# Kernel tuning notes

Measured on AMD Instinct MI355X. Metric: run time of the kernel, lower is better.

## Reference

```python
import jax, jax.numpy as jnp
import numpy as np

T_DIL = 10   # neighbor-count threshold
K_DIL = 2    # skip hyperparameter
BN_EPS = 1e-5
NORM_EPS = 1e-12


def _dilate_pattern(adj_bool, mask_b):
    """Sequential (row-by-row) dilated neighbor skipping on a [N,N] bool adjacency.
    Faithful to the torch double loop: earlier rows' removals (including the
    symmetric column zeroing) affect later rows' neighbor sets."""
    N = adj_bool.shape[0]

    def step(carry, n):
        row = jnp.take(carry, n, axis=0)                 # [N] bool, current neighbors of n
        nbi = row.astype(jnp.int32)
        num = jnp.sum(nbi)
        sf = jnp.where(num > T_DIL, (num + K_DIL - 1) // K_DIL, 1)  # linear mode, ceil(num/k)
        rank = jnp.cumsum(nbi)                           # 1-based rank among neighbors
        rm = row & ((rank % sf) == 0)                    # neighbors[sf-1::sf]
        valid = (mask_b[n] != 0) & (num > 1)
        rm = jnp.where(valid, rm, False)
        keep = ~rm
        carry = carry.at[n].set(row & keep)              # adj[n, to_remove] = 0
        carry = carry.at[:, n].set(carry[:, n] & keep)   # adj[to_remove, n] = 0
        return carry, None

    out, _ = jax.lax.scan(step, adj_bool, jnp.arange(N))
    return out


def _dilate(adj, mask):
    # keep-pattern is piecewise constant in adj; multiply so removed entries -> 0
    keep = jax.vmap(_dilate_pattern)(adj > 0, mask)
    return adj * keep.astype(adj.dtype)


def _sage(x, adj, Wr, Wx, b, mf):
    # DenseSAGEConv: mean-aggregate, lin_rel + lin_root, L2 normalize, mask
    deg = jnp.clip(jnp.sum(adj, axis=-1, keepdims=True), 1.0, None)
    agg = jnp.einsum('bij,bjd->bid', adj, x) / deg
    out = agg @ Wr + x @ Wx + b
    nrm = jnp.maximum(jnp.linalg.norm(out, axis=-1, keepdims=True), NORM_EPS)
    return (out / nrm) * mf[..., None]


def _bn(x, g, b):
    # BatchNorm1d in training mode over flattened (B*N) rows, biased variance
    m = jnp.mean(x, axis=(0, 1))
    v = jnp.var(x, axis=(0, 1))
    return (x - m) * jax.lax.rsqrt(v + BN_EPS) * g + b


def _forward(x, adj, mask, Wr1, Wx1, b1, g1, be1, Wr2, Wx2, b2, g2, be2,
             Wr3, Wx3, b3, g3, be3, Wl, bl):
    mf = mask.astype(x.dtype)
    # linear dilation mode: skip factor is layer-independent, and each layer
    # dilates the ORIGINAL adj (torch clones adj per call) -> compute once
    adj_d = _dilate(adj, mask)
    h1 = _bn(jax.nn.relu(_sage(x, adj_d, Wr1, Wx1, b1, mf)), g1, be1)
    h2 = _bn(jax.nn.relu(_sage(h1, adj_d, Wr2, Wx2, b2, mf)), g2, be2)
    h3 = _bn(jax.nn.relu(_sage(h2, adj_d, Wr3, Wx3, b3, mf)), g3, be3)
    xc = jnp.concatenate([h1, h2, h3], axis=-1) * mf[..., None]
    return (xc @ Wl + bl) * mf[..., None]


def setup_inputs() -> dict:
    B, N, D, H, E = 8, 2048, 128, 128, 128
    key = jax.random.key(0)
    ks = jax.random.split(key, 24)
    x = jax.random.normal(ks[0], (B, N, D), dtype=jnp.float32)
    a = jax.random.bernoulli(ks[1], 0.01, (B, N, N))
    a = a | jnp.swapaxes(a, 1, 2)
    a = a & ~jnp.eye(N, dtype=bool)[None]
    adj = a.astype(jnp.float32)
    mask = jnp.ones((B, N), dtype=jnp.int32)
    s = 0.05
    p = {}
    dims = [(D, H), (H, H), (H, E)]
    for i, (di, do) in enumerate(dims, 1):
        p[f'Wr{i}'] = s * jax.random.normal(ks[2 * i], (di, do), dtype=jnp.float32)
        p[f'Wx{i}'] = s * jax.random.normal(ks[2 * i + 1], (di, do), dtype=jnp.float32)
        p[f'b{i}'] = jnp.zeros((do,), dtype=jnp.float32)
        p[f'g{i}'] = jnp.ones((do,), dtype=jnp.float32)
        p[f'be{i}'] = jnp.zeros((do,), dtype=jnp.float32)
    p['Wl'] = s * jax.random.normal(ks[10], (2 * H + E, E), dtype=jnp.float32)
    p['bl'] = jnp.zeros((E,), dtype=jnp.float32)
    return {'x': x, 'adj': adj, 'mask': mask, **p}


def reference(x, adj, mask, Wr1, Wx1, b1, g1, be1, Wr2, Wx2, b2, g2, be2,
              Wr3, Wx3, b3, g3, be3, Wl, bl):
    return _forward(x, adj, mask, Wr1, Wx1, b1, g1, be1, Wr2, Wx2, b2, g2, be2,
                    Wr3, Wx3, b3, g3, be3, Wl, bl)
```

## Files before the change

kernel.cpp:

```cpp
#include <hip/hip_runtime.h>
#include <cstdint>

constexpr int B_ = 8, N_ = 2048, D_ = 128, NW = 64;
constexpr int EMAX = 131072;
constexpr int RPS = 2064;
constexpr int TDIL = 10;

constexpr size_t OFF_BITSET = 0;
constexpr size_t OFF_AGG    = 0;
constexpr size_t OFF_H1     = (size_t)8  << 20;
constexpr size_t OFF_H2     = (size_t)16 << 20;
constexpr size_t OFF_H3     = (size_t)24 << 20;
constexpr size_t OFF_XB     = (size_t)24 << 20;
constexpr size_t OFF_H1B    = (size_t)28 << 20;
constexpr size_t OFF_H2B    = (size_t)24 << 20;
constexpr size_t OFF_COLS   = (size_t)32 << 20;
constexpr size_t OFF_PACKED = (size_t)34 << 20;
constexpr size_t OFF_RP     = (size_t)38 << 20;
constexpr size_t OFF_DEG0   = OFF_RP   + ((size_t)128 << 10);
constexpr size_t OFF_DEGF   = OFF_DEG0 + ((size_t)64  << 10);
constexpr size_t OFF_BN     = OFF_DEGF + ((size_t)64  << 10);
constexpr size_t OFF_WHI    = OFF_BN  + ((size_t)4 << 10);
constexpr size_t OFF_WLO    = OFF_WHI + ((size_t)304 << 10);

typedef __attribute__((ext_vector_type(8))) short short8v;
typedef __attribute__((ext_vector_type(4))) float f32x4;

__device__ __forceinline__ uint16_t bf16rne(float f) {
    uint32_t u = __float_as_uint(f);
    return (uint16_t)((u + 0x7FFFu + ((u >> 16) & 1u)) >> 16);
}

__global__ __launch_bounds__(256) void kW_prep(
        const float* __restrict__ Wr1, const float* __restrict__ Wx1,
        const float* __restrict__ Wr2, const float* __restrict__ Wx2,
        const float* __restrict__ Wr3, const float* __restrict__ Wx3,
        const float* __restrict__ Wl,
        uint16_t* __restrict__ whi, uint16_t* __restrict__ wlo,
        float* __restrict__ bn,
        const float* __restrict__ x, uint16_t* __restrict__ xb) {
    if (blockIdx.x >= 128) {
        size_t i = ((size_t)(blockIdx.x - 128) * 256 + threadIdx.x) * 4;
        float4 v = *(const float4*)&x[i];
        ushort4 o;
        o.x = bf16rne(v.x); o.y = bf16rne(v.y);
        o.z = bf16rne(v.z); o.w = bf16rne(v.w);
        *(ushort4*)&xb[i] = o;
        return;
    }
    if (blockIdx.x == 0) {
        for (int i = threadIdx.x; i < 768; i += 256) bn[i] = 0.f;
    }
    int g  = blockIdx.x >> 5;
    int lb = blockIdx.x & 31;
    int K = (g == 3) ? 384 : 256;
    const float* A  = (g == 0) ? Wr1 : (g == 1) ? Wr2 : (g == 2) ? Wr3 : Wl;
    const float* Bw = (g == 0) ? Wx1 : (g == 1) ? Wx2 : (g == 2) ? Wx3 : nullptr;
    size_t base = (g == 3) ? (size_t)98304 : (size_t)g * 32768;
    int total = K * 128;
    for (int f = lb * 256 + threadIdx.x; f < total; f += 32 * 256) {
        int e = f & 7, lane = (f >> 3) & 63, ct = (f >> 9) & 7, ks = f >> 12;
        int k = ks * 32 + ((lane >> 4) << 3) + e;
        int col = (ct << 4) + (lane & 15);
        float v = (g == 3 || k < 128) ? A[(size_t)k * 128 + col]
                                      : Bw[(size_t)(k - 128) * 128 + col];
        uint32_t hi = bf16rne(v);
        float hf = __uint_as_float(hi << 16);
        whi[base + f] = (uint16_t)hi;
        wlo[base + f] = bf16rne(v - hf);
    }
}

__global__ __launch_bounds__(256) void k1_bitset(const float* __restrict__ adj,
        uint32_t* __restrict__ bitset, uint32_t* __restrict__ deg0) {
    int row  = blockIdx.x * 4 + (threadIdx.x >> 6);
    int lane = threadIdx.x & 63;
    const float* ar = adj + (size_t)row * N_;
    uint32_t myw = 0;
    #pragma unroll 4
    for (int it = 0; it < 32; ++it) {
        float v = ar[it * 64 + lane];
        unsigned long long m = __ballot(v != 0.0f);
        if (lane == 2 * it)          myw = (uint32_t)m;
        else if (lane == 2 * it + 1) myw = (uint32_t)(m >> 32);
    }
    bitset[(size_t)row * NW + lane] = myw;
    int pc = __popc(myw);
    #pragma unroll
    for (int off = 32; off >= 1; off >>= 1) pc += __shfl_xor(pc, off);
    if (lane == 0) deg0[row] = (uint32_t)pc;
}

__global__ __launch_bounds__(256) void k2_rowptr(const uint32_t* __restrict__ deg0,
        uint32_t* __restrict__ rowptr) {
    int b = blockIdx.x, t = threadIdx.x;
    __shared__ uint32_t tsum[256];
    uint32_t v[8]; uint32_t s = 0;
    #pragma unroll
    for (int j = 0; j < 8; ++j) { v[j] = deg0[b * N_ + t * 8 + j]; s += v[j]; v[j] = s; }
    tsum[t] = s;
    __syncthreads();
    for (int off = 1; off < 256; off <<= 1) {
        uint32_t xv = (t >= off) ? tsum[t - off] : 0u;
        __syncthreads();
        tsum[t] += xv;
        __syncthreads();
    }
    uint32_t excl = tsum[t] - s;
    uint32_t* rp = rowptr + (size_t)b * RPS;
    if (t == 0) rp[0] = 0;
    #pragma unroll
    for (int j = 0; j < 8; ++j) {
        uint32_t val = excl + v[j];
        if (val > (uint32_t)EMAX) val = EMAX;
        rp[t * 8 + j + 1] = val;
    }
}

__global__ __launch_bounds__(256) void k3_cols(const uint32_t* __restrict__ bitset,
        const uint32_t* __restrict__ rowptr, uint16_t* __restrict__ cols) {
    int row  = blockIdx.x * 4 + (threadIdx.x >> 6);
    int lane = threadIdx.x & 63;
    int b = row >> 11, n = row & (N_ - 1);
    uint32_t w = bitset[(size_t)row * NW + lane];
    uint32_t pc = __popc(w);
    uint32_t inc = pc;
    #pragma unroll
    for (int off = 1; off < 64; off <<= 1) {
        uint32_t t = __shfl_up(inc, off);
        if (lane >= off) inc += t;
    }
    uint32_t base = rowptr[(size_t)b * RPS + n] + (inc - pc);
    uint16_t* cb = cols + (size_t)b * EMAX;
    while (w) {
        int bit = __builtin_ctz(w); w &= w - 1;
        if (base < (uint32_t)EMAX) cb[base] = (uint16_t)(lane * 32 + bit);
        ++base;
    }
}

__global__ __launch_bounds__(256) void k4_packed(const uint16_t* __restrict__ cols,
        const uint32_t* __restrict__ rowptr, uint32_t* __restrict__ packed) {
    int row  = blockIdx.x * 4 + (threadIdx.x >> 6);
    int lane = threadIdx.x & 63;
    int b = row >> 11, n = row & (N_ - 1);
    const uint32_t* rpb = rowptr + (size_t)b * RPS;
    const uint16_t* cb  = cols + (size_t)b * EMAX;
    uint32_t start = rpb[n], end = rpb[n + 1];
    for (uint32_t e = start + lane; e < end; e += 64) {
        uint32_t j = cb[e];
        uint32_t lo = rpb[j], hi = rpb[j + 1];
        uint32_t rj = lo;
        while (lo < hi) {
            uint32_t mid = (lo + hi) >> 1;
            if ((int)cb[mid] < n) lo = mid + 1; else hi = mid;
        }
        packed[(size_t)b * EMAX + e] = j | ((lo - rj) << 16);
    }
}

#define K5_ISSUE(PK0, PK1, CNT, ROW)                                        \
    do {                                                                    \
        int rr_ = (ROW);                                                    \
        if (rr_ < N_) {                                                     \
            uint32_t ldI_ = rps[rr_], enI_ = rps[rr_ + 1];                  \
            CNT = (int)(enI_ - ldI_);                                       \
            PK0 = (lane < CNT) ? pkg[ldI_ + lane] : 0xFFFFFFFFu;            \
            if (CNT > 64)                                                   \
                PK1 = (lane + 64 < CNT) ? pkg[ldI_ + 64 + lane] : 0xFFFFFFFFu; \
            else PK1 = 0xFFFFFFFFu;                                         \
        } else { CNT = 0; PK0 = 0xFFFFFFFFu; PK1 = 0xFFFFFFFFu; }           \
    } while (0)

#define K5_PROC(PK0, PK1, CNT, NROW)                                        \
    do {                                                                    \
        int nr_ = (NROW);                                                   \
        if (CNT <= 64) {                                                    \
                            \
            uint32_t c0_ = PK0 & 0xFFFFu;                                   \
            bool e0_ = (lane < CNT) && (c0_ < (uint32_t)nr_);               \
            while (true) {                                                  \
                uint32_t d0_ = e0_ ? __hip_atomic_load(&done[c0_ >> 5],     \
                        __ATOMIC_ACQUIRE, __HIP_MEMORY_SCOPE_WORKGROUP) : 0u; \
                bool ok0_ = !e0_ || ((d0_ >> (c0_ & 31)) & 1u);             \
                if (__all((int)ok0_)) break;                                \
            }                                                               \
            __builtin_amdgcn_s_setprio(1);                                  \
            uint2 mc_ = *(const uint2*)&rm4[(size_t)nr_ * 4];               \
            uint32_t w01_ = (lane < 32) ? mc_.x : mc_.y;                    \
            uint32_t a0_ = (w01_ >> (lane & 31)) & 1u;                      \
            unsigned long long bl0_ = __ballot(a0_ != 0);                   \
            uint32_t num_ = (uint32_t)__popcll(bl0_);                       \
            if (mk[nr_] && num_ > 1u) {                                     \
                bool allrm_ = num_ <= (uint32_t)TDIL;                       \
                uint32_t sf_ = (num_ + 1u) >> 1;                            \
                uint32_t r2_ = (num_ & 1u) ? 0xFFFFFFFFu : num_;            \
                uint32_t rank0_ = (uint32_t)__popcll(bl0_ & below) + 1u;    \
                bool rm0_ = a0_ && (allrm_ || rank0_ == sf_ || rank0_ == r2_); \
                unsigned long long rb0_ = __ballot(rm0_);                   \
                if (rm0_) {                                                 \
                    uint32_t ml_ = PK0 >> 16;                               \
                    if (ml_ < 128u) atomicAnd(&rm4[c0_ * 4 + (ml_ >> 5)], ~(1u << (ml_ & 31))); \
                }                                                           \
                if (lane == 0) {                                            \
                    uint2 nm_;                                              \
                    nm_.x = mc_.x & ~(uint32_t)rb0_;                        \
                    nm_.y = mc_.y & ~(uint32_t)(rb0_ >> 32);                \
                    *(uint2*)&rm4[(size_t)nr_ * 4] = nm_;                   \
                }                                                           \
            }                                                               \
            __asm__ __volatile__("" ::: "memory");                          \
            if (lane == 0)                                                  \
                __hip_atomic_fetch_or(&done[nr_ >> 5], 1u << (nr_ & 31),    \
                        __ATOMIC_RELAXED, __HIP_MEMORY_SCOPE_WORKGROUP);    \
            __builtin_amdgcn_s_setprio(0);                                  \
        } else {                                                            \
                      \
            uint32_t c0_ = PK0 & 0xFFFFu, c1_ = PK1 & 0xFFFFu;              \
            bool e0_ = (lane < CNT)      && (c0_ < (uint32_t)nr_);          \
            bool e1_ = (lane + 64 < CNT) && (c1_ < (uint32_t)nr_);          \
            while (true) {                                                  \
                uint32_t d0_ = e0_ ? __hip_atomic_load(&done[c0_ >> 5],     \
                        __ATOMIC_ACQUIRE, __HIP_MEMORY_SCOPE_WORKGROUP) : 0u; \
                uint32_t d1_ = e1_ ? __hip_atomic_load(&done[c1_ >> 5],     \
                        __ATOMIC_ACQUIRE, __HIP_MEMORY_SCOPE_WORKGROUP) : 0u; \
                bool ok0_ = !e0_ || ((d0_ >> (c0_ & 31)) & 1u);             \
                bool ok1_ = !e1_ || ((d1_ >> (c1_ & 31)) & 1u);             \
                if (__all((int)(ok0_ && ok1_))) break;                      \
            }                                                               \
            __builtin_amdgcn_s_setprio(1);                                  \
            uint4 mcur_ = *(const uint4*)&rm4[(size_t)nr_ * 4];             \
            uint32_t w01_ = (lane < 32) ? mcur_.x : mcur_.y;                \
            uint32_t w23_ = (lane < 32) ? mcur_.z : mcur_.w;                \
            uint32_t a0_ = (w01_ >> (lane & 31)) & 1u;                      \
            uint32_t a1_ = (w23_ >> (lane & 31)) & 1u;                      \
            unsigned long long bl0_ = __ballot(a0_ != 0), bl1_ = __ballot(a1_ != 0); \
            uint32_t num_ = (uint32_t)__popcll(bl0_) + (uint32_t)__popcll(bl1_); \
            if (mk[nr_] && num_ > 1u) {                                     \
                bool allrm_ = num_ <= (uint32_t)TDIL;                       \
                uint32_t sf_ = (num_ + 1u) >> 1;                            \
                uint32_t r2_ = (num_ & 1u) ? 0xFFFFFFFFu : num_;            \
                uint32_t rank0_ = (uint32_t)__popcll(bl0_ & below) + 1u;    \
                uint32_t rank1_ = (uint32_t)__popcll(bl0_) +                \
                                  (uint32_t)__popcll(bl1_ & below) + 1u;    \
                bool rm0_ = a0_ && (allrm_ || rank0_ == sf_ || rank0_ == r2_); \
                bool rm1_ = a1_ && (allrm_ || rank1_ == sf_ || rank1_ == r2_); \
                unsigned long long rb0_ = __ballot(rm0_), rb1_ = __ballot(rm1_); \
                if (rm0_) {                                                 \
                    uint32_t ml_ = PK0 >> 16;                               \
                    if (ml_ < 128u) atomicAnd(&rm4[c0_ * 4 + (ml_ >> 5)], ~(1u << (ml_ & 31))); \
                }                                                           \
                if (rm1_) {                                                 \
                    uint32_t ml_ = PK1 >> 16;                               \
                    if (ml_ < 128u) atomicAnd(&rm4[c1_ * 4 + (ml_ >> 5)], ~(1u << (ml_ & 31))); \
                }                                                           \
                if (lane == 0) {                                            \
                    uint4 nm_;                                              \
                    nm_.x = mcur_.x & ~(uint32_t)rb0_;                      \
                    nm_.y = mcur_.y & ~(uint32_t)(rb0_ >> 32);              \
                    nm_.z = mcur_.z & ~(uint32_t)rb1_;                      \
                    nm_.w = mcur_.w & ~(uint32_t)(rb1_ >> 32);              \
                    *(uint4*)&rm4[(size_t)nr_ * 4] = nm_;                   \
                }                                                           \
            }                                                               \
            __asm__ __volatile__("" ::: "memory");                          \
            if (lane == 0)                                                  \
                __hip_atomic_fetch_or(&done[nr_ >> 5], 1u << (nr_ & 31),    \
                        __ATOMIC_RELAXED, __HIP_MEMORY_SCOPE_WORKGROUP);    \
            __builtin_amdgcn_s_setprio(0);                                  \
        }                                                                   \
    } while (0)

__global__ __launch_bounds__(1024) void k5_fused(
        const uint32_t* __restrict__ packed, const uint32_t* __restrict__ rowptr,
        const uint32_t* __restrict__ deg0, const int* __restrict__ mask,
        uint16_t* __restrict__ cols, uint32_t* __restrict__ degf) {
    int b = blockIdx.x;
    int tid = threadIdx.x;
    int lane = tid & 63;
    int wv = tid >> 6;
    __shared__ __align__(16) uint32_t rm4[N_ * 4];
    __shared__ uint32_t rps[N_ + 1];
    __shared__ uint8_t  mk[N_];
    __shared__ uint32_t done[64];
    const uint32_t* pkg = packed + (size_t)b * EMAX;
    const uint32_t* rpg = rowptr + (size_t)b * RPS;
    uint16_t* cbm = cols + (size_t)b * EMAX;

    for (int i = tid; i <= N_; i += 1024) rps[i] = rpg[i];
    if (tid < 64) done[tid] = 0u;
    for (int i = tid; i < N_; i += 1024) {
        int d = (int)deg0[b * N_ + i]; if (d > 128) d = 128;
        uint4 mm;
        mm.x = (d >= 32) ? ~0u : ((d > 0)  ? ((1u << d)        - 1u) : 0u);
        mm.y = (d >= 64) ? ~0u : ((d > 32) ? ((1u << (d - 32)) - 1u) : 0u);
        mm.z = (d >= 96) ? ~0u : ((d > 64) ? ((1u << (d - 64)) - 1u) : 0u);
        mm.w = (d >= 128)? ~0u : ((d > 96) ? ((1u << (d - 96)) - 1u) : 0u);
        *(uint4*)&rm4[(size_t)i * 4] = mm;
        mk[i] = (uint8_t)(mask[b * N_ + i] != 0);
    }
    __syncthreads();

    unsigned long long below = (1ULL << lane) - 1ULL;
    int cntA, cntB, cntC;
    uint32_t pkA0, pkA1, pkB0, pkB1, pkC0, pkC1;
    K5_ISSUE(pkA0, pkA1, cntA, wv);
    K5_ISSUE(pkB0, pkB1, cntB, wv + 16);
    K5_ISSUE(pkC0, pkC1, cntC, wv + 32);

    int n = wv;
    while (n < N_) {
        K5_PROC(pkA0, pkA1, cntA, n);
        K5_ISSUE(pkA0, pkA1, cntA, n + 48);
        n += 16; if (n >= N_) break;
        K5_PROC(pkB0, pkB1, cntB, n);
        K5_ISSUE(pkB0, pkB1, cntB, n + 48);
        n += 16; if (n >= N_) break;
        K5_PROC(pkC0, pkC1, cntC, n);
        K5_ISSUE(pkC0, pkC1, cntC, n + 48);
        n += 16;
    }
    __syncthreads();

    for (int i = wv; i < N_; i += 16) {
        uint4 mm = *(const uint4*)&rm4[(size_t)i * 4];
        if (lane == 0)
            degf[b * N_ + i] = (uint32_t)(__popc(mm.x) + __popc(mm.y) +
                                          __popc(mm.z) + __popc(mm.w));
        uint32_t st = rps[i];
        uint32_t w01 = (lane < 32) ? mm.x : mm.y;
        uint32_t w23 = (lane < 32) ? mm.z : mm.w;
        uint32_t a0 = (w01 >> (lane & 31)) & 1u;
        uint32_t a1 = (w23 >> (lane & 31)) & 1u;
        unsigned long long b0 = __ballot(a0 != 0), b1v = __ballot(a1 != 0);
        uint16_t c0v = 0, c1v = 0;
        if (a0) c0v = cbm[st + lane];
        if (a1) c1v = cbm[st + 64 + lane];
        uint32_t i0 = st + (uint32_t)__popcll(b0 & below);
        uint32_t i1 = st + (uint32_t)__popcll(b0) + (uint32_t)__popcll(b1v & below);
        if (a0) cbm[i0] = c0v;
        if (a1) cbm[i1] = c1v;
    }
}

__global__ __launch_bounds__(256) void k7_spmm(const uint16_t* __restrict__ Xb16,
        const uint16_t* __restrict__ cols, const uint32_t* __restrict__ rowptr,
        const uint32_t* __restrict__ degf, float* __restrict__ agg) {
    int wid  = blockIdx.x * 4 + (threadIdx.x >> 6);
    int lane = threadIdx.x & 63;
    int b = wid >> 11, n = wid & (N_ - 1);
    const uint16_t* cb = cols + (size_t)b * EMAX;
    uint32_t start = rowptr[(size_t)b * RPS + n];
    uint32_t cnt = degf[wid];
    const uint16_t* Xb = Xb16 + ((size_t)b * N_) * D_;
    float ax = 0.f, ay = 0.f;
    for (uint32_t base = 0; base < cnt; base += 64) {
        int idx = (int)base + lane;
        int cl = (idx < (int)cnt) ? (int)cb[start + idx] : 0;
        int kmax = (int)cnt - (int)base; if (kmax > 64) kmax = 64;
        int k = 0;
        for (; k + 4 <= kmax; k += 4) {
            int cA = __shfl(cl, k),     cB = __shfl(cl, k + 1);
            int cC = __shfl(cl, k + 2), cD = __shfl(cl, k + 3);
            uint32_t uA = ((const uint32_t*)(Xb + (size_t)cA * D_))[lane];
            uint32_t uB = ((const uint32_t*)(Xb + (size_t)cB * D_))[lane];
            uint32_t uC = ((const uint32_t*)(Xb + (size_t)cC * D_))[lane];
            uint32_t uD = ((const uint32_t*)(Xb + (size_t)cD * D_))[lane];
            ax += __uint_as_float(uA << 16) + __uint_as_float(uB << 16)
                + __uint_as_float(uC << 16) + __uint_as_float(uD << 16);
            ay += __uint_as_float(uA & 0xFFFF0000u) + __uint_as_float(uB & 0xFFFF0000u)
                + __uint_as_float(uC & 0xFFFF0000u) + __uint_as_float(uD & 0xFFFF0000u);
        }
        for (; k < kmax; ++k) {
            int c = __shfl(cl, k);
            uint32_t u = ((const uint32_t*)(Xb + (size_t)c * D_))[lane];
            ax += __uint_as_float(u << 16);
            ay += __uint_as_float(u & 0xFFFF0000u);
        }
    }
    float inv = 1.0f / (float)(cnt ? cnt : 1u);
    ((float2*)(agg + (size_t)wid * D_))[lane] = make_float2(ax * inv, ay * inv);
}

__device__ __forceinline__ void cvt_store4(uint16_t* hiA, uint16_t* loA,
                                           int idx, float4 v) {
    float vv[4] = {v.x, v.y, v.z, v.w};
    ushort4 hs, ls;
    uint16_t* hp = (uint16_t*)&hs; uint16_t* lp = (uint16_t*)&ls;
    #pragma unroll
    for (int i = 0; i < 4; ++i) {
        uint32_t hi = bf16rne(vv[i]);
        float hf = __uint_as_float(hi << 16);
        hp[i] = (uint16_t)hi;
        lp[i] = bf16rne(vv[i] - hf);
    }
    *(ushort4*)&hiA[idx] = hs;
    *(ushort4*)&loA[idx] = ls;
}

constexpr int ASTR = 264;
__global__ __launch_bounds__(256) void k8_mfma(const float* __restrict__ agg,
        const float* __restrict__ Hin,
        const uint16_t* __restrict__ whi, const uint16_t* __restrict__ wlo,
        const float* __restrict__ bias, const int* __restrict__ mask,
        const float* __restrict__ bnp, const float* __restrict__ gp,
        const float* __restrict__ bep, int use_bn,
        float* __restrict__ P, uint16_t* __restrict__ Pb,
        float* __restrict__ bnstat) {
    __shared__ __align__(16) char buf[2 * 32 * ASTR * 2];
    __shared__ float scL[128], shL[128];
    uint16_t* aHi = (uint16_t*)buf;
    uint16_t* aLo = (uint16_t*)(buf + 32 * ASTR * 2);
    float* outP = (float*)buf;
    int tid = threadIdx.x, lane = tid & 63, h = tid >> 6;
    size_t row0 = (size_t)blockIdx.x * 32;

    if (tid < 128) {
        float sc = 1.f, sh = 0.f;
        if (use_bn) {
            float mean = bnp[tid] * (1.f / 16384.f);
            float var  = bnp[128 + tid] * (1.f / 16384.f) - mean * mean;
            sc = gp[tid] * rsqrtf(var + 1e-5f);
            sh = bep[tid] - mean * sc;
        }
        scL[tid] = sc; shL[tid] = sh;
    }
    __syncthreads();

    for (int f = tid * 4; f < 4096; f += 1024) {
        int r = f >> 7, c = f & 127;
        float4 va = *(const float4*)&agg[(row0 + r) * 128 + c];
        float4 vx = *(const float4*)&Hin[(row0 + r) * 128 + c];
        float4 s4 = *(const float4*)&scL[c];
        float4 h4 = *(const float4*)&shL[c];
        va.x = va.x * s4.x + h4.x; va.y = va.y * s4.y + h4.y;
        va.z = va.z * s4.z + h4.z; va.w = va.w * s4.w + h4.w;
        vx.x = vx.x * s4.x + h4.x; vx.y = vx.y * s4.y + h4.y;
        vx.z = vx.z * s4.z + h4.z; vx.w = vx.w * s4.w + h4.w;
        cvt_store4(aHi, aLo, r * ASTR + c, va);
        cvt_store4(aHi, aLo, r * ASTR + 128 + c, vx);
    }
    __syncthreads();

    f32x4 acc00 = {0.f,0.f,0.f,0.f}, acc01 = acc00, acc10 = acc00, acc11 = acc00;
    int ct0 = h * 2, ct1 = h * 2 + 1;
    int arow = (lane & 15);
    int koff = (lane >> 4) * 8;
    #pragma unroll
    for (int ks = 0; ks < 8; ++ks) {
        int k0 = ks * 32 + koff;
        short8v a0h = *(short8v*)&aHi[arow * ASTR + k0];
        short8v a0l = *(short8v*)&aLo[arow * ASTR + k0];
        short8v a1h = *(short8v*)&aHi[(arow + 16) * ASTR + k0];
        short8v a1l = *(short8v*)&aLo[(arow + 16) * ASTR + k0];
        short8v b0h = *(const short8v*)&whi[(size_t)(((ks * 8 + ct0) << 6) + lane) * 8];
        short8v b0l = *(const short8v*)&wlo[(size_t)(((ks * 8 + ct0) << 6) + lane) * 8];
        short8v b1h = *(const short8v*)&whi[(size_t)(((ks * 8 + ct1) << 6) + lane) * 8];
        short8v b1l = *(const short8v*)&wlo[(size_t)(((ks * 8 + ct1) << 6) + lane) * 8];
        acc00 = __builtin_amdgcn_mfma_f32_16x16x32_bf16(a0h, b0h, acc00, 0, 0, 0);
        acc00 = __builtin_amdgcn_mfma_f32_16x16x32_bf16(a0h, b0l, acc00, 0, 0, 0);
        acc00 = __builtin_amdgcn_mfma_f32_16x16x32_bf16(a0l, b0h, acc00, 0, 0, 0);
        acc01 = __builtin_amdgcn_mfma_f32_16x16x32_bf16(a0h, b1h, acc01, 0, 0, 0);
        acc01 = __builtin_amdgcn_mfma_f32_16x16x32_bf16(a0h, b1l, acc01, 0, 0, 0);
        acc01 = __builtin_amdgcn_mfma_f32_16x16x32_bf16(a0l, b1h, acc01, 0, 0, 0);
        acc10 = __builtin_amdgcn_mfma_f32_16x16x32_bf16(a1h, b0h, acc10, 0, 0, 0);
        acc10 = __builtin_amdgcn_mfma_f32_16x16x32_bf16(a1h, b0l, acc10, 0, 0, 0);
        acc10 = __builtin_amdgcn_mfma_f32_16x16x32_bf16(a1l, b0h, acc10, 0, 0, 0);
        acc11 = __builtin_amdgcn_mfma_f32_16x16x32_bf16(a1h, b1h, acc11, 0, 0, 0);
        acc11 = __builtin_amdgcn_mfma_f32_16x16x32_bf16(a1h, b1l, acc11, 0, 0, 0);
        acc11 = __builtin_amdgcn_mfma_f32_16x16x32_bf16(a1l, b1h, acc11, 0, 0, 0);
    }
    __syncthreads();

    int orow = (lane >> 4) * 4;
    int oc0 = ct0 * 16 + (lane & 15);
    int oc1 = ct1 * 16 + (lane & 15);
    #pragma unroll
    for (int j = 0; j < 4; ++j) {
        outP[(orow + j) * 128 + oc0]      = acc00[j];
        outP[(orow + j) * 128 + oc1]      = acc01[j];
        outP[(16 + orow + j) * 128 + oc0] = acc10[j];
        outP[(16 + orow + j) * 128 + oc1] = acc11[j];
    }
    __syncthreads();

    float bs0 = bias[lane], bs1 = bias[lane + 64];
    #pragma unroll
    for (int i = 0; i < 8; ++i) {
        int r = h * 8 + i;
        float v0 = outP[r * 128 + lane] + bs0;
        float v1 = outP[r * 128 + lane + 64] + bs1;
        float s = v0 * v0 + v1 * v1;
        #pragma unroll
        for (int off = 32; off >= 1; off >>= 1) s += __shfl_xor(s, off);
        float nrm = fmaxf(sqrtf(s), 1e-12f);
        float mf = (mask[row0 + r] != 0) ? 1.f : 0.f;
        float inv = mf / nrm;
        float p0 = fmaxf(v0 * inv, 0.f), p1 = fmaxf(v1 * inv, 0.f);
        P[(row0 + r) * 128 + lane]      = p0;
        P[(row0 + r) * 128 + lane + 64] = p1;
        if (Pb) {
            Pb[(row0 + r) * 128 + lane]      = bf16rne(p0);
            Pb[(row0 + r) * 128 + lane + 64] = bf16rne(p1);
        }
        outP[r * 128 + lane] = p0; outP[r * 128 + lane + 64] = p1;
    }
    __syncthreads();
    if (tid < 128) {
        float s = 0.f, q = 0.f;
        #pragma unroll
        for (int r = 0; r < 32; ++r) { float v = outP[r * 128 + tid]; s += v; q += v * v; }
        atomicAdd(&bnstat[tid], s);
        atomicAdd(&bnstat[128 + tid], q);
    }
}

__global__ __launch_bounds__(256) void k11_final(const float* __restrict__ h1,
        const float* __restrict__ h2, const float* __restrict__ h3,
        const float* __restrict__ Wl, const float* __restrict__ bl,
        const int* __restrict__ mask, const float* __restrict__ bn,
        const float* __restrict__ g1, const float* __restrict__ be1,
        const float* __restrict__ g2, const float* __restrict__ be2,
        const float* __restrict__ g3, const float* __restrict__ be3,
        float* __restrict__ out) {
    __shared__ float s1[32 * 128], s2[32 * 128], s3[32 * 128];
    __shared__ float scA[128], shA[128], scB[128], shB[128], scC[128], shC[128];
    int tid = threadIdx.x;
    size_t row0 = (size_t)blockIdx.x * 32;
    if (tid < 128) {
        float m1 = bn[tid] * (1.f / 16384.f);
        float v1 = bn[128 + tid] * (1.f / 16384.f) - m1 * m1;
        scA[tid] = g1[tid] * rsqrtf(v1 + 1e-5f);
        shA[tid] = be1[tid] - m1 * scA[tid];
        float m2 = bn[256 + tid] * (1.f / 16384.f);
        float v2 = bn[384 + tid] * (1.f / 16384.f) - m2 * m2;
        scB[tid] = g2[tid] * rsqrtf(v2 + 1e-5f);
        shB[tid] = be2[tid] - m2 * scB[tid];
        float m3 = bn[512 + tid] * (1.f / 16384.f);
        float v3 = bn[640 + tid] * (1.f / 16384.f) - m3 * m3;
        scC[tid] = g3[tid] * rsqrtf(v3 + 1e-5f);
        shC[tid] = be3[tid] - m3 * scC[tid];
    }
    __syncthreads();
    for (int t = tid * 4; t < 32 * 128; t += 1024) {
        int r = t >> 7;
        float mf = (mask[row0 + r] != 0) ? 1.f : 0.f;
        int c = t & 127;
        float4 a = *(const float4*)&h1[row0 * 128 + t];
        float4 b = *(const float4*)&h2[row0 * 128 + t];
        float4 cc = *(const float4*)&h3[row0 * 128 + t];
        float4 sa = *(const float4*)&scA[c], ha = *(const float4*)&shA[c];
        float4 sb = *(const float4*)&scB[c], hb = *(const float4*)&shB[c];
        float4 sc = *(const float4*)&scC[c], hc = *(const float4*)&shC[c];
        a.x = (a.x * sa.x + ha.x) * mf; a.y = (a.y * sa.y + ha.y) * mf;
        a.z = (a.z * sa.z + ha.z) * mf; a.w = (a.w * sa.w + ha.w) * mf;
        b.x = (b.x * sb.x + hb.x) * mf; b.y = (b.y * sb.y + hb.y) * mf;
        b.z = (b.z * sb.z + hb.z) * mf; b.w = (b.w * sb.w + hb.w) * mf;
        cc.x = (cc.x * sc.x + hc.x) * mf; cc.y = (cc.y * sc.y + hc.y) * mf;
        cc.z = (cc.z * sc.z + hc.z) * mf; cc.w = (cc.w * sc.w + hc.w) * mf;
        *(float4*)&s1[t] = a; *(float4*)&s2[t] = b; *(float4*)&s3[t] = cc;
    }
    __syncthreads();
    int h = tid >> 6, c0 = (tid & 63) * 2;
    float2 acc[8];
    #pragma unroll
    for (int i = 0; i < 8; ++i) acc[i] = make_float2(0.f, 0.f);
    for (int k4 = 0; k4 < 128; k4 += 4) {
        float2 w1[4], w2[4], w3[4];
        #pragma unroll
        for (int kk = 0; kk < 4; ++kk) {
            w1[kk] = *(const float2*)&Wl[(k4 + kk) * 128 + c0];
            w2[kk] = *(const float2*)&Wl[(128 + k4 + kk) * 128 + c0];
            w3[kk] = *(const float2*)&Wl[(256 + k4 + kk) * 128 + c0];
        }
        #pragma unroll
        for (int i = 0; i < 8; ++i) {
            int r = h * 8 + i;
            float4 a = *(const float4*)&s1[r * 128 + k4];
            float4 b = *(const float4*)&s2[r * 128 + k4];
            float4 c = *(const float4*)&s3[r * 128 + k4];
            acc[i].x += a.x * w1[0].x + a.y * w1[1].x + a.z * w1[2].x + a.w * w1[3].x
                      + b.x * w2[0].x + b.y * w2[1].x + b.z * w2[2].x + b.w * w2[3].x
                      + c.x * w3[0].x + c.y * w3[1].x + c.z * w3[2].x + c.w * w3[3].x;
            acc[i].y += a.x * w1[0].y + a.y * w1[1].y + a.z * w1[2].y + a.w * w1[3].y
                      + b.x * w2[0].y + b.y * w2[1].y + b.z * w2[2].y + b.w * w2[3].y
                      + c.x * w3[0].y + c.y * w3[1].y + c.z * w3[2].y + c.w * w3[3].y;
        }
    }
    float bx = bl[c0], by = bl[c0 + 1];
    #pragma unroll
    for (int i = 0; i < 8; ++i) {
        int r = h * 8 + i;
        float mf = (mask[row0 + r] != 0) ? 1.f : 0.f;
        *(float2*)&out[(row0 + r) * 128 + c0] =
            make_float2((acc[i].x + bx) * mf, (acc[i].y + by) * mf);
    }
}

extern "C" void kernel_launch(void* const* d_in, const int* in_sizes, int n_in,
                              void* d_out, int out_size, void* d_ws, size_t ws_size,
                              hipStream_t stream) {
    (void)in_sizes; (void)n_in; (void)out_size; (void)ws_size;
    const float* x    = (const float*)d_in[0];
    const float* adj  = (const float*)d_in[1];
    const int*   mask = (const int*)d_in[2];
    const float* Wr1 = (const float*)d_in[3],  *Wx1 = (const float*)d_in[4];
    const float* b1  = (const float*)d_in[5],  *g1  = (const float*)d_in[6],  *be1 = (const float*)d_in[7];
    const float* Wr2 = (const float*)d_in[8],  *Wx2 = (const float*)d_in[9];
    const float* b2  = (const float*)d_in[10], *g2  = (const float*)d_in[11], *be2 = (const float*)d_in[12];
    const float* Wr3 = (const float*)d_in[13], *Wx3 = (const float*)d_in[14];
    const float* b3  = (const float*)d_in[15], *g3  = (const float*)d_in[16], *be3 = (const float*)d_in[17];
    const float* Wl  = (const float*)d_in[18], *bl  = (const float*)d_in[19];

    char* ws = (char*)d_ws;
    uint32_t* bitset = (uint32_t*)(ws + OFF_BITSET);
    float*    agg    = (float*)(ws + OFF_AGG);
    float*    h1     = (float*)(ws + OFF_H1);
    float*    h2     = (float*)(ws + OFF_H2);
    float*    h3     = (float*)(ws + OFF_H3);
    uint16_t* xb     = (uint16_t*)(ws + OFF_XB);
    uint16_t* h1b    = (uint16_t*)(ws + OFF_H1B);
    uint16_t* h2b    = (uint16_t*)(ws + OFF_H2B);
    uint16_t* cols   = (uint16_t*)(ws + OFF_COLS);
    uint32_t* packed = (uint32_t*)(ws + OFF_PACKED);
    uint32_t* rp     = (uint32_t*)(ws + OFF_RP);
    uint32_t* deg0   = (uint32_t*)(ws + OFF_DEG0);
    uint32_t* degf   = (uint32_t*)(ws + OFF_DEGF);
    float*    bn     = (float*)(ws + OFF_BN);
    uint16_t* whi    = (uint16_t*)(ws + OFF_WHI);
    uint16_t* wlo    = (uint16_t*)(ws + OFF_WLO);
    float*    out    = (float*)d_out;

    kW_prep   <<<2176, 256, 0, stream>>>(Wr1, Wx1, Wr2, Wx2, Wr3, Wx3, Wl,
                                         whi, wlo, bn, x, xb);
    k1_bitset <<<4096, 256, 0, stream>>>(adj, bitset, deg0);
    k2_rowptr <<<8,    256, 0, stream>>>(deg0, rp);
    k3_cols   <<<4096, 256, 0, stream>>>(bitset, rp, cols);
    k4_packed <<<4096, 256, 0, stream>>>(cols, rp, packed);
    k5_fused  <<<8,    1024, 0, stream>>>(packed, rp, deg0, mask, cols, degf);
    k7_spmm   <<<4096, 256, 0, stream>>>(xb,  cols, rp, degf, agg);
    k8_mfma   <<<512,  256, 0, stream>>>(agg, x,  whi,         wlo,         b1, mask,
                                         bn, g1, be1, 0, h1, h1b, bn + 0);
    k7_spmm   <<<4096, 256, 0, stream>>>(h1b, cols, rp, degf, agg);
    k8_mfma   <<<512,  256, 0, stream>>>(agg, h1, whi + 32768, wlo + 32768, b2, mask,
                                         bn + 0, g1, be1, 1, h2, h2b, bn + 256);
    k7_spmm   <<<4096, 256, 0, stream>>>(h2b, cols, rp, degf, agg);
    k8_mfma   <<<512,  256, 0, stream>>>(agg, h2, whi + 65536, wlo + 65536, b3, mask,
                                         bn + 256, g2, be2, 1, h3, nullptr, bn + 512);
    k11_final <<<512,  256, 0, stream>>>(h1, h2, h3, Wl, bl, mask, bn,
                                         g1, be1, g2, be2, g3, be3, out);
}
```

Measured before the change: 330.3 us.

## Replace column compaction in dilate kernel with per-row keep bitmask consumed by SpMM

The dilate kernel no longer compacts the surviving columns into the CSR column array. It writes each row's 128-bit keep mask to global memory, and the SpMM kernel walks the original CSR row while skipping entries whose mask bit is clear. This removes the serial-ish compaction tail from the single-block-per-batch dilate kernel. The cost is that the SpMM inner loop loses its 4-way unrolling and now runs a per-entry branch over the undilated degree, three times.

After: 359.3 us. 1.09x slower.

```diff
diff --git a/kernel.cpp b/kernel.cpp
--- a/kernel.cpp
+++ b/kernel.cpp
@@ -19,7 +19,8 @@
 constexpr size_t OFF_RP     = (size_t)38 << 20;
 constexpr size_t OFF_DEG0   = OFF_RP   + ((size_t)128 << 10);
 constexpr size_t OFF_DEGF   = OFF_DEG0 + ((size_t)64  << 10);
-constexpr size_t OFF_BN     = OFF_DEGF + ((size_t)64  << 10);
+constexpr size_t OFF_RMASK  = OFF_DEGF + ((size_t)64  << 10);
+constexpr size_t OFF_BN     = OFF_RMASK + ((size_t)256 << 10);
 constexpr size_t OFF_WHI    = OFF_BN  + ((size_t)4 << 10);
 constexpr size_t OFF_WLO    = OFF_WHI + ((size_t)304 << 10);
 
@@ -271,10 +272,10 @@
         }                                                                   \
     } while (0)
 
-__global__ __launch_bounds__(1024) void k5_fused(
+__global__ __launch_bounds__(1024) void k5_dilate(
         const uint32_t* __restrict__ packed, const uint32_t* __restrict__ rowptr,
         const uint32_t* __restrict__ deg0, const int* __restrict__ mask,
-        uint16_t* __restrict__ cols, uint32_t* __restrict__ degf) {
+        uint32_t* __restrict__ rmaskg, uint32_t* __restrict__ degf) {
     int b = blockIdx.x;
     int tid = threadIdx.x;
     int lane = tid & 63;
@@ -285,7 +286,6 @@
     __shared__ uint32_t done[64];
     const uint32_t* pkg = packed + (size_t)b * EMAX;
     const uint32_t* rpg = rowptr + (size_t)b * RPS;
-    uint16_t* cbm = cols + (size_t)b * EMAX;
 
     for (int i = tid; i <= N_; i += 1024) rps[i] = rpg[i];
     if (tid < 64) done[tid] = 0u;
@@ -321,63 +321,44 @@
         n += 16;
     }
     __syncthreads();
-
-    for (int i = wv; i < N_; i += 16) {
+    for (int i = tid; i < N_; i += 1024) {
         uint4 mm = *(const uint4*)&rm4[(size_t)i * 4];
-        if (lane == 0)
-            degf[b * N_ + i] = (uint32_t)(__popc(mm.x) + __popc(mm.y) +
-                                          __popc(mm.z) + __popc(mm.w));
-        uint32_t st = rps[i];
-        uint32_t w01 = (lane < 32) ? mm.x : mm.y;
-        uint32_t w23 = (lane < 32) ? mm.z : mm.w;
-        uint32_t a0 = (w01 >> (lane & 31)) & 1u;
-        uint32_t a1 = (w23 >> (lane & 31)) & 1u;
-        unsigned long long b0 = __ballot(a0 != 0), b1v = __ballot(a1 != 0);
-        uint16_t c0v = 0, c1v = 0;
-        if (a0) c0v = cbm[st + lane];
-        if (a1) c1v = cbm[st + 64 + lane];
-        uint32_t i0 = st + (uint32_t)__popcll(b0 & below);
-        uint32_t i1 = st + (uint32_t)__popcll(b0) + (uint32_t)__popcll(b1v & below);
-        if (a0) cbm[i0] = c0v;
-        if (a1) cbm[i1] = c1v;
+        *(uint4*)&rmaskg[((size_t)b * N_ + i) * 4] = mm;
+        degf[b * N_ + i] = (uint32_t)(__popc(mm.x) + __popc(mm.y) + __popc(mm.z) + __popc(mm.w));
     }
 }
 
 __global__ __launch_bounds__(256) void k7_spmm(const uint16_t* __restrict__ Xb16,
         const uint16_t* __restrict__ cols, const uint32_t* __restrict__ rowptr,
-        const uint32_t* __restrict__ degf, float* __restrict__ agg) {
+        const uint32_t* __restrict__ rmaskg, const uint32_t* __restrict__ degf,
+        float* __restrict__ agg) {
     int wid  = blockIdx.x * 4 + (threadIdx.x >> 6);
     int lane = threadIdx.x & 63;
     int b = wid >> 11, n = wid & (N_ - 1);
     const uint16_t* cb = cols + (size_t)b * EMAX;
     uint32_t start = rowptr[(size_t)b * RPS + n];
-    uint32_t cnt = degf[wid];
+    uint32_t end   = rowptr[(size_t)b * RPS + n + 1];
+    int cnt0 = (int)(end - start);
+    uint4 mm = *(const uint4*)&rmaskg[(size_t)wid * 4];
+    unsigned long long am0 = (unsigned long long)mm.x | ((unsigned long long)mm.y << 32);
+    unsigned long long am1 = (unsigned long long)mm.z | ((unsigned long long)mm.w << 32);
     const uint16_t* Xb = Xb16 + ((size_t)b * N_) * D_;
     float ax = 0.f, ay = 0.f;
-    for (uint32_t base = 0; base < cnt; base += 64) {
-        int idx = (int)base + lane;
-        int cl = (idx < (int)cnt) ? (int)cb[start + idx] : 0;
-        int kmax = (int)cnt - (int)base; if (kmax > 64) kmax = 64;
-        int k = 0;
-        for (; k + 4 <= kmax; k += 4) {
-            int cA = __shfl(cl, k),     cB = __shfl(cl, k + 1);
-            int cC = __shfl(cl, k + 2), cD = __shfl(cl, k + 3);
-            uint32_t uA = ((const uint32_t*)(Xb + (size_t)cA * D_))[lane];
-            uint32_t uB = ((const uint32_t*)(Xb + (size_t)cB * D_))[lane];
-            uint32_t uC = ((const uint32_t*)(Xb + (size_t)cC * D_))[lane];
-            uint32_t uD = ((const uint32_t*)(Xb + (size_t)cD * D_))[lane];
-            ax += __uint_as_float(uA << 16) + __uint_as_float(uB << 16)
-                + __uint_as_float(uC << 16) + __uint_as_float(uD << 16);
-            ay += __uint_as_float(uA & 0xFFFF0000u) + __uint_as_float(uB & 0xFFFF0000u)
-                + __uint_as_float(uC & 0xFFFF0000u) + __uint_as_float(uD & 0xFFFF0000u);
+    for (int base = 0; base < cnt0; base += 64) {
+        int idx = base + lane;
+        int cl = (idx < cnt0) ? (int)cb[start + idx] : 0;
+        unsigned long long am = base ? am1 : am0;
+        int kmax = cnt0 - base; if (kmax > 64) kmax = 64;
+        for (int k = 0; k < kmax; ++k) {
+            if ((am >> k) & 1ULL) {
+                int c = __shfl(cl, k);
+                uint32_t u = ((const uint32_t*)(Xb + (size_t)c * D_))[lane];
+                ax += __uint_as_float(u << 16);
+                ay += __uint_as_float(u & 0xFFFF0000u);
+            }
         }
-        for (; k < kmax; ++k) {
-            int c = __shfl(cl, k);
-            uint32_t u = ((const uint32_t*)(Xb + (size_t)c * D_))[lane];
-            ax += __uint_as_float(u << 16);
-            ay += __uint_as_float(u & 0xFFFF0000u);
-        }
-    }
+    }
+    uint32_t cnt = degf[wid];
     float inv = 1.0f / (float)(cnt ? cnt : 1u);
     ((float2*)(agg + (size_t)wid * D_))[lane] = make_float2(ax * inv, ay * inv);
 }
@@ -626,6 +607,7 @@
     uint32_t* rp     = (uint32_t*)(ws + OFF_RP);
     uint32_t* deg0   = (uint32_t*)(ws + OFF_DEG0);
     uint32_t* degf   = (uint32_t*)(ws + OFF_DEGF);
+    uint32_t* rmaskg = (uint32_t*)(ws + OFF_RMASK);
     float*    bn     = (float*)(ws + OFF_BN);
     uint16_t* whi    = (uint16_t*)(ws + OFF_WHI);
     uint16_t* wlo    = (uint16_t*)(ws + OFF_WLO);
@@ -637,14 +619,14 @@
     k2_rowptr <<<8,    256, 0, stream>>>(deg0, rp);
     k3_cols   <<<4096, 256, 0, stream>>>(bitset, rp, cols);
     k4_packed <<<4096, 256, 0, stream>>>(cols, rp, packed);
-    k5_fused  <<<8,    1024, 0, stream>>>(packed, rp, deg0, mask, cols, degf);
-    k7_spmm   <<<4096, 256, 0, stream>>>(xb,  cols, rp, degf, agg);
+    k5_dilate <<<8,    1024, 0, stream>>>(packed, rp, deg0, mask, rmaskg, degf);
+    k7_spmm   <<<4096, 256, 0, stream>>>(xb,  cols, rp, rmaskg, degf, agg);
     k8_mfma   <<<512,  256, 0, stream>>>(agg, x,  whi,         wlo,         b1, mask,
                                          bn, g1, be1, 0, h1, h1b, bn + 0);
-    k7_spmm   <<<4096, 256, 0, stream>>>(h1b, cols, rp, degf, agg);
+    k7_spmm   <<<4096, 256, 0, stream>>>(h1b, cols, rp, rmaskg, degf, agg);
     k8_mfma   <<<512,  256, 0, stream>>>(agg, h1, whi + 32768, wlo + 32768, b2, mask,
                                          bn + 0, g1, be1, 1, h2, h2b, bn + 256);
-    k7_spmm   <<<4096, 256, 0, stream>>>(h2b, cols, rp, degf, agg);
+    k7_spmm   <<<4096, 256, 0, stream>>>(h2b, cols, rp, rmaskg, degf, agg);
     k8_mfma   <<<512,  256, 0, stream>>>(agg, h2, whi + 65536, wlo + 65536, b3, mask,
                                          bn + 256, g2, be2, 1, h3, nullptr, bn + 512);
     k11_final <<<512,  256, 0, stream>>>(h1, h2, h3, Wl, bl, mask, bn,
```
